# Optimization experiments

Measured on AMD Instinct MI355X. Metric: run time of the kernel, lower is better.

Reference implementation:

```python
import jax, jax.numpy as jnp
import numpy as np

B = 2048
DIMS = [300, 74, 35]
R = 3
ENC = 150
HID = 32
CAT = ENC * R  # 450


def setup_inputs() -> dict:
    key = jax.random.key(0)
    ks = jax.random.split(key, 32)
    d = {}
    for i, dim in enumerate(DIMS):
        d[f"x{i}"] = jax.random.normal(ks[i], (B, 1, dim), dtype=jnp.float32)
    s = 0.05
    for i, dim in enumerate(DIMS):
        d[f"encW{i}"] = jax.random.normal(ks[3 + 2 * i], (ENC, dim), dtype=jnp.float32) * s
        d[f"encb{i}"] = jax.random.normal(ks[4 + 2 * i], (ENC,), dtype=jnp.float32) * s
    d["affw"] = jax.random.normal(ks[10], (R,), dtype=jnp.float32) * s      # Linear(1,1) weight per branch
    d["Ww"] = jax.random.normal(ks[11], (R, HID, 1), dtype=jnp.float32) * s  # Linear(1,32)
    d["Wc"] = jax.random.normal(ks[12], (R, HID, CAT), dtype=jnp.float32) * s  # Linear(450,32)
    d["Wh"] = jax.random.normal(ks[13], (R, 1, HID), dtype=jnp.float32) * s   # Linear(32,1)
    d["clsW1"] = jax.random.normal(ks[14], (128, CAT), dtype=jnp.float32) * s
    d["clsb1"] = jax.random.normal(ks[15], (128,), dtype=jnp.float32) * s
    d["clsW2"] = jax.random.normal(ks[16], (7, 128), dtype=jnp.float32) * s
    d["clsb2"] = jax.random.normal(ks[17], (7,), dtype=jnp.float32) * s
    return d


def reference(x0, x1, x2, encW0, encb0, encW1, encb1, encW2, encb2,
              affw, Ww, Wc, Wh, clsW1, clsb1, clsW2, clsb2):
    xs = [x0, x1, x2]
    encW = [encW0, encW1, encW2]
    encb = [encb0, encb1, encb2]
    # Encode each modality: [B,1,dim_i] -> [B,1,150]
    enc = [jnp.einsum('btd,ed->bte', xs[i], encW[i]) + encb[i] for i in range(R)]
    feat_n = jnp.concatenate(enc, axis=2)            # [B,1,450]
    scale = 1.0 / jnp.sqrt(jnp.float32(feat_n.shape[1]))  # T=1
    att_feats = []
    for i in range(R):
        enc_t = jnp.swapaxes(enc[i], 1, 2)           # [B,150,1]
        t = jnp.swapaxes(feat_n, 1, 2) * affw[i]     # [B,450,1] (Linear(1,1), no bias)
        # outer product attention: [B,150,1] @ [B,1,450] -> [B,150,450]
        att = jnp.tanh(jnp.matmul(enc_t, jnp.swapaxes(t, 1, 2)) * scale)
        a = jnp.einsum('bec,hc->beh', att, Wc[i])    # [B,150,32]
        b = jnp.matmul(enc_t, Ww[i].T)               # [B,150,1]@[1,32] -> [B,150,32]
        H = jax.nn.relu(a + b)
        out_i = jnp.swapaxes(jnp.matmul(H, Wh[i].T), 1, 2) + enc[i]  # [B,1,150]
        att_feats.append(out_i)
    feats = jnp.concatenate(att_feats, axis=2)       # [B,1,450]
    # classifier (dropout is identity in eval mode)
    h = jnp.einsum('btc,kc->btk', feats, clsW1) + clsb1
    return jnp.einsum('btk,ok->bto', h, clsW2) + clsb2
```

## Files before the change

### kernel.cpp

```cpp
#include <hip/hip_runtime.h>
#include <math.h>

#define NJ 5
#define DEG 9
#define X0f 1.25f
#define NB 8
#define NT 768

struct Poly { float c[NJ]; };

#define FMA4(A,S,W) do { (A).x = fmaf((S),(W).x,(A).x); (A).y = fmaf((S),(W).y,(A).y); \
                         (A).z = fmaf((S),(W).z,(A).z); (A).w = fmaf((S),(W).w,(A).w); } while(0)

__global__ __launch_bounds__(256) void k_repack(
    const float* __restrict__ Wc, const float* __restrict__ W1,
    const float* __restrict__ eW0, const float* __restrict__ eW1, const float* __restrict__ eW2,
    float* __restrict__ WcT, float* __restrict__ W1T,
    float* __restrict__ Wt0, float* __restrict__ Wt1, float* __restrict__ Wt2) {
    int tid = blockIdx.x * 256 + threadIdx.x;
    int stride = gridDim.x * 256;
    for (int idx = tid; idx < 3 * 464 * 32; idx += stride) {
        int i = idx / (464 * 32); int rem = idx - i * 464 * 32;
        int m = rem >> 5, h = rem & 31;
        float v = 0.f;
        if (m < 456) {
            int seg = m / 152, e = m - seg * 152;
            if (e < 150) v = Wc[((size_t)i * 32 + h) * 450 + seg * 150 + e];
        }
        WcT[idx] = v;
    }
    for (int idx = tid; idx < 456 * 128; idx += stride) {
        int m = idx >> 7, k = idx & 127;
        int seg = m / 152, e = m - seg * 152;
        W1T[idx] = (e < 150) ? W1[k * 450 + seg * 150 + e] : 0.f;
    }
    for (int idx = tid; idx < 304 * 152; idx += stride) {
        int d = idx / 152, e = idx - d * 152;
        Wt0[idx] = (d < 300 && e < 150) ? eW0[e * 300 + d] : 0.f;
    }
    for (int idx = tid; idx < 76 * 152; idx += stride) {
        int d = idx / 152, e = idx - d * 152;
        Wt1[idx] = (d < 74 && e < 150) ? eW1[e * 74 + d] : 0.f;
    }
    for (int idx = tid; idx < 36 * 152; idx += stride) {
        int d = idx / 152, e = idx - d * 152;
        Wt2[idx] = (d < 35 && e < 150) ? eW2[e * 35 + d] : 0.f;
    }
}

__global__ __launch_bounds__(NT, 1) void k_fused(
    const float* __restrict__ x0, const float* __restrict__ x1, const float* __restrict__ x2,
    const float* __restrict__ eb0, const float* __restrict__ eb1, const float* __restrict__ eb2,
    const float* __restrict__ Wt0, const float* __restrict__ Wt1, const float* __restrict__ Wt2,
    const float* __restrict__ WcT,
    const float* __restrict__ affw, const float* __restrict__ Ww, const float* __restrict__ Wh,
    const float* __restrict__ W1T, const float* __restrict__ cb1,
    const float* __restrict__ cW2, const float* __restrict__ cb2,
    float* __restrict__ out, Poly pc) {
    __shared__ __align__(16) float xs[NB * 428];
    __shared__ __align__(16) float featf[NB * 468];
    __shared__ __align__(16) float fof[NB * 468];
    __shared__ __align__(16) float wWs[96], wHs[96];

    int tid = threadIdx.x;
    int b0 = blockIdx.x * NB;

    if (tid < 96) { wWs[tid] = Ww[tid]; wHs[tid] = Wh[tid]; }
    if (tid >= 96 && tid < 192) {
        int q = tid - 96; int b = q / 12, r = q - b * 12;
        featf[b * 468 + 456 + r] = 0.f;
    }
    if (tid >= 192 && tid < 240) {
        int q = tid - 192; int b = q / 6, r = q - b * 6;
        fof[b * 468 + (r >> 1) * 152 + 150 + (r & 1)] = 0.f;
    }
    for (int idx = tid; idx < NB * 75; idx += NT) {
        int b = idx / 75, q = idx - b * 75;
        ((float4*)(xs + b * 428))[q] = ((const float4*)(x0 + (size_t)(b0 + b) * 300))[q];
    }
    for (int idx = tid; idx < NB * 74; idx += NT) {
        int b = idx / 74, d = idx - b * 74;
        xs[b * 428 + 304 + d] = x1[(size_t)(b0 + b) * 74 + d];
    }
    for (int idx = tid; idx < NB * 35; idx += NT) {
        int b = idx / 35, d = idx - b * 35;
        xs[b * 428 + 380 + d] = x2[(size_t)(b0 + b) * 35 + d];
    }
    __syncthreads();

    {
        int tasks[2]; int nt = 1;
        tasks[0] = tid;
        if (tid >= 624) { tasks[nt++] = 768 + (767 - tid); }
        for (int q = 0; q < nt; ++q) {
            int task = tasks[q];
            int b = task & 7, m4 = task >> 3;
            int seg = (m4 >= 76) ? 2 : (m4 >= 38) ? 1 : 0;
            int e4 = m4 - seg * 38;
            const float* eb = seg == 0 ? eb0 : seg == 1 ? eb1 : eb2;
            const float4* Wt4 = (const float4*)(seg == 0 ? Wt0 : seg == 1 ? Wt1 : Wt2) + e4;
            const float* xb = xs + b * 428 + (seg == 0 ? 0 : seg == 1 ? 304 : 380);
            int DP4 = seg == 0 ? 76 : seg == 1 ? 19 : 9;
            const float4* xr = (const float4*)xb;
            int e = e4 * 4;
            float4 acc;
            acc.x = (e     < 150) ? eb[e]     : 0.f;
            acc.y = (e + 1 < 150) ? eb[e + 1] : 0.f;
            acc.z = (e + 2 < 150) ? eb[e + 2] : 0.f;
            acc.w = (e + 3 < 150) ? eb[e + 3] : 0.f;
            for (int d4 = 0; d4 < DP4; ++d4) {
                float4 x4 = xr[d4];
                float4 w0 = Wt4[(d4 * 4 + 0) * 38];
                float4 w1 = Wt4[(d4 * 4 + 1) * 38];
                float4 w2 = Wt4[(d4 * 4 + 2) * 38];
                float4 w3 = Wt4[(d4 * 4 + 3) * 38];
                FMA4(acc, x4.x, w0);
                FMA4(acc, x4.y, w1);
                FMA4(acc, x4.z, w2);
                FMA4(acc, x4.w, w3);
            }
            ((float4*)(featf + b * 468))[m4] = acc;
        }
    }
    __syncthreads();

    {
        int w = tid >> 6;
        int i = w >> 2, wp = w & 3;
        int lane = tid & 63;
        int hq = lane & 7, slice = (lane >> 3) & 3, bh = lane >> 5;
        int b = wp * 2 + bh;
        float aff = affw[i];
        const float4* Wb4 = (const float4*)WcT + (size_t)i * 3712 + hq;
        const float4* frow = (const float4*)(featf + b * 468);

        float4 acc[NJ];
        #pragma unroll
        for (int J = 0; J < NJ; ++J) acc[J] = make_float4(0.f, 0.f, 0.f, 0.f);
        float mx = 0.f;

        int m4lo = slice * 29;
        #pragma unroll 2
        for (int m4 = m4lo; m4 < m4lo + 29; ++m4) {
            float4 f4 = frow[m4];
            const float4* wp4 = Wb4 + m4 * 32;
            float4 w0 = wp4[0];
            float4 w1 = wp4[8];
            float4 w2 = wp4[16];
            float4 w3 = wp4[24];
            mx = fmaxf(mx, fmaxf(fmaxf(fabsf(f4.x), fabsf(f4.y)), fmaxf(fabsf(f4.z), fabsf(f4.w))));
            float g0 = aff * f4.x, g1 = aff * f4.y, g2 = aff * f4.z, g3 = aff * f4.w;
            float q0 = g0 * g0, q1 = g1 * g1, q2 = g2 * g2, q3 = g3 * g3;
            float p0 = g0, p1 = g1, p2 = g2, p3 = g3;
            FMA4(acc[0], p0, w0); FMA4(acc[0], p1, w1); FMA4(acc[0], p2, w2); FMA4(acc[0], p3, w3);
            #pragma unroll
            for (int J = 1; J < NJ; ++J) {
                p0 *= q0; p1 *= q1; p2 *= q2; p3 *= q3;
                FMA4(acc[J], p0, w0); FMA4(acc[J], p1, w1); FMA4(acc[J], p2, w2); FMA4(acc[J], p3, w3);
            }
        }
        #pragma unroll
        for (int J = 0; J < NJ; ++J) {
            float cJ = pc.c[J];
            float vx = acc[J].x; vx += __shfl_xor(vx, 8); vx += __shfl_xor(vx, 16);
            float vy = acc[J].y; vy += __shfl_xor(vy, 8); vy += __shfl_xor(vy, 16);
            float vz = acc[J].z; vz += __shfl_xor(vz, 8); vz += __shfl_xor(vz, 16);
            float vw = acc[J].w; vw += __shfl_xor(vw, 8); vw += __shfl_xor(vw, 16);
            acc[J].x = vx * cJ; acc[J].y = vy * cJ; acc[J].z = vz * cJ; acc[J].w = vw * cJ;
        }
        mx = fmaxf(mx, __shfl_xor(mx, 1));
        mx = fmaxf(mx, __shfl_xor(mx, 2));
        mx = fmaxf(mx, __shfl_xor(mx, 4));
        mx = fmaxf(mx, __shfl_xor(mx, 8));
        mx = fmaxf(mx, __shfl_xor(mx, 16));
        float gmax = fabsf(aff) * mx;

        float4 wW4 = ((const float4*)wWs)[i * 8 + hq];
        float4 wH4 = ((const float4*)wHs)[i * 8 + hq];
        int e4lo = slice * 10;
        int e4hi = (slice == 3) ? 38 : (e4lo + 10);
        for (int e4 = e4lo; e4 < e4hi; ++e4) {
            float4 s4 = frow[i * 38 + e4];
            float ores[4];
            #pragma unroll
            for (int r = 0; r < 4; ++r) {
                float s = (r == 0) ? s4.x : (r == 1) ? s4.y : (r == 2) ? s4.z : s4.w;
                float4 a4;
                if (fabsf(s) * gmax <= X0f) {
                    float s2 = s * s, p = s;
                    a4.x = acc[0].x * p; a4.y = acc[0].y * p;
                    a4.z = acc[0].z * p; a4.w = acc[0].w * p;
                    #pragma unroll
                    for (int J = 1; J < NJ; ++J) { p *= s2; FMA4(a4, p, acc[J]); }
                } else {
                    a4 = make_float4(0.f, 0.f, 0.f, 0.f);
                    for (int c = 0; c < 456; ++c) {
                        float t = tanhf(s * aff * featf[b * 468 + c]);
                        float4 wv = Wb4[c * 8];
                        FMA4(a4, t, wv);
                    }
                }
                float hx = fmaxf(fmaf(s, wW4.x, a4.x), 0.f);
                float hy = fmaxf(fmaf(s, wW4.y, a4.y), 0.f);
                float hz = fmaxf(fmaf(s, wW4.z, a4.z), 0.f);
                float hw = fmaxf(fmaf(s, wW4.w, a4.w), 0.f);
                float csum = hx * wH4.x + hy * wH4.y + hz * wH4.z + hw * wH4.w;
                csum += __shfl_xor(csum, 1);
                csum += __shfl_xor(csum, 2);
                csum += __shfl_xor(csum, 4);
                ores[r] = csum + s;
            }
            if (hq == 0)
                ((float4*)(fof + b * 468))[i * 38 + e4] = make_float4(ores[0], ores[1], ores[2], ores[3]);
        }
    }
    __syncthreads();

    {
        int cs = tid >> 8;
        int rr = tid & 255;
        int b = rr & 7, k4 = rr >> 3;
        const float4* W14 = (const float4*)W1T + k4;
        const float4* fr = (const float4*)(fof + b * 468);
        float4 a = make_float4(0.f, 0.f, 0.f, 0.f);
        int c4lo = cs * 38;
        for (int c4 = c4lo; c4 < c4lo + 38; ++c4) {
            float4 fv = fr[c4];
            float4 w0 = W14[(c4 * 4 + 0) * 32];
            float4 w1 = W14[(c4 * 4 + 1) * 32];
            float4 w2 = W14[(c4 * 4 + 2) * 32];
            float4 w3 = W14[(c4 * 4 + 3) * 32];
            FMA4(a, fv.x, w0);
            FMA4(a, fv.y, w1);
            FMA4(a, fv.z, w2);
            FMA4(a, fv.w, w3);
        }
        ((float4*)xs)[(cs * 8 + b) * 33 + k4] = a;
    }
    __syncthreads();
    if (tid < 256) {
        int b = tid >> 5, k4 = tid & 31;
        const float4* hp4 = (const float4*)xs;
        float4 v  = hp4[(0 * 8 + b) * 33 + k4];
        float4 v1 = hp4[(1 * 8 + b) * 33 + k4];
        float4 v2 = hp4[(2 * 8 + b) * 33 + k4];
        float4 bias = ((const float4*)cb1)[k4];
        v.x += v1.x + v2.x + bias.x;
        v.y += v1.y + v2.y + bias.y;
        v.z += v1.z + v2.z + bias.z;
        v.w += v1.w + v2.w + bias.w;
        ((float4*)(featf + b * 468))[k4] = v;
    }
    __syncthreads();
    if (tid < NB * 7) {
        int b = tid / 7, o = tid - (tid / 7) * 7;
        const float* hb = featf + b * 468;
        const float* w2 = cW2 + o * 128;
        float acc = cb2[o];
        #pragma unroll 4
        for (int k = 0; k < 128; ++k) acc = fmaf(hb[k], w2[k], acc);
        out[(size_t)(b0 + b) * 7 + o] = acc;
    }
}

static void make_poly(float* cf) {
    const double a = 1.25;
    const int NQ = 128;
    const double PI = 3.14159265358979323846;
    double b[DEG + 1];
    for (int k = 0; k <= DEG; ++k) b[k] = 0.0;
    for (int m = 0; m < NQ; ++m) {
        double th = PI * (m + 0.5) / NQ;
        double f = tanh(a * cos(th));
        for (int k = 1; k <= DEG; k += 2)
            b[k] += (2.0 / NQ) * f * cos(k * th);
    }
    double Tp[DEG + 1], Tc[DEG + 1], Tn[DEG + 1], mono[DEG + 1];
    for (int j = 0; j <= DEG; ++j) { Tp[j] = 0; Tc[j] = 0; mono[j] = 0; }
    Tp[0] = 1.0;
    Tc[1] = 1.0;
    for (int j = 0; j <= DEG; ++j) mono[j] += b[1] * Tc[j];
    for (int k = 2; k <= DEG; ++k) {
        for (int j = 0; j <= DEG; ++j) Tn[j] = -Tp[j];
        for (int j = 1; j <= DEG; ++j) Tn[j] += 2.0 * Tc[j - 1];
        for (int j = 0; j <= DEG; ++j) { Tp[j] = Tc[j]; Tc[j] = Tn[j]; }
        if (k & 1) for (int j = 0; j <= DEG; ++j) mono[j] += b[k] * Tc[j];
    }
    for (int J = 0; J < NJ; ++J) {
        int j = 2 * J + 1;
        cf[J] = (float)(mono[j] / pow(a, (double)j));
    }
}

extern "C" void kernel_launch(void* const* d_in, const int* in_sizes, int n_in,
                              void* d_out, int out_size, void* d_ws, size_t ws_size,
                              hipStream_t stream) {
    (void)in_sizes; (void)n_in; (void)out_size; (void)ws_size;
    const float* x0    = (const float*)d_in[0];
    const float* x1    = (const float*)d_in[1];
    const float* x2    = (const float*)d_in[2];
    const float* eW0   = (const float*)d_in[3];
    const float* eb0   = (const float*)d_in[4];
    const float* eW1   = (const float*)d_in[5];
    const float* eb1   = (const float*)d_in[6];
    const float* eW2   = (const float*)d_in[7];
    const float* eb2   = (const float*)d_in[8];
    const float* affw  = (const float*)d_in[9];
    const float* Ww    = (const float*)d_in[10];
    const float* Wc    = (const float*)d_in[11];
    const float* Wh    = (const float*)d_in[12];
    const float* cW1   = (const float*)d_in[13];
    const float* cb1   = (const float*)d_in[14];
    const float* cW2   = (const float*)d_in[15];
    const float* cb2   = (const float*)d_in[16];

    float* ws    = (float*)d_ws;
    float* wsWcT = ws;
    float* wsW1T = ws + 44544;
    float* wsWt0 = ws + 102912;
    float* wsWt1 = ws + 149120;
    float* wsWt2 = ws + 160672;

    Poly pc;
    make_poly(pc.c);

    k_repack<<<dim3(96), dim3(256), 0, stream>>>(Wc, cW1, eW0, eW1, eW2,
                                                 wsWcT, wsW1T, wsWt0, wsWt1, wsWt2);
    k_fused<<<dim3(256), dim3(NT), 0, stream>>>(x0, x1, x2, eb0, eb1, eb2,
                                                wsWt0, wsWt1, wsWt2, wsWcT,
                                                affw, Ww, Wh, wsW1T, cb1, cW2, cb2,
                                                (float*)d_out, pc);
}
```

Baseline: 67.29 us.

## Share Wc loads across two batch rows and shrink tanh polynomial degree

Each lane in the moment-accumulation loop now processes two batch rows at once, so every loaded Wc weight float4 serves both rows. The feature range is split eight ways instead of four, and an extra shuffle stage reduces across the wider split. The tanh Chebyshev polynomial degree drops from 9 to 7 and the accuracy threshold from 1.25 to 1.1, cutting the accumulator count. The trade-off is more inputs falling back to the exact tanh loop, more register pressure, and some loss of accuracy.

```diff
diff --git a/kernel.cpp b/kernel.cpp
--- a/kernel.cpp
+++ b/kernel.cpp
@@ -1,9 +1,9 @@
 #include <hip/hip_runtime.h>
 #include <math.h>
 
-#define NJ 5
-#define DEG 9
-#define X0f 1.25f
+#define NJ 4
+#define DEG 7
+#define X0f 1.1f
 #define NB 8
 #define NT 768
 
@@ -128,57 +128,93 @@
         int w = tid >> 6;
         int i = w >> 2, wp = w & 3;
         int lane = tid & 63;
-        int hq = lane & 7, slice = (lane >> 3) & 3, bh = lane >> 5;
-        int b = wp * 2 + bh;
+        int hq = lane & 7, slice = lane >> 3;
+        int slice2 = (lane >> 3) & 3, bh = lane >> 5;
         float aff = affw[i];
         const float4* Wb4 = (const float4*)WcT + (size_t)i * 3712 + hq;
-        const float4* frow = (const float4*)(featf + b * 468);
-
-        float4 acc[NJ];
+        int bA = wp * 2, bB = bA + 1;
+        const float4* frowA = (const float4*)(featf + bA * 468);
+        const float4* frowB = (const float4*)(featf + bB * 468);
+
+        float4 accA[NJ], accB[NJ];
         #pragma unroll
-        for (int J = 0; J < NJ; ++J) acc[J] = make_float4(0.f, 0.f, 0.f, 0.f);
-        float mx = 0.f;
-
-        int m4lo = slice * 29;
-        #pragma unroll 2
-        for (int m4 = m4lo; m4 < m4lo + 29; ++m4) {
-            float4 f4 = frow[m4];
+        for (int J = 0; J < NJ; ++J) {
+            accA[J] = make_float4(0.f, 0.f, 0.f, 0.f);
+            accB[J] = make_float4(0.f, 0.f, 0.f, 0.f);
+        }
+        float mxA = 0.f, mxB = 0.f;
+
+        int m4lo = (slice < 4) ? slice * 15 : 60 + (slice - 4) * 14;
+        int m4n  = (slice < 4) ? 15 : 14;
+        #pragma unroll 3
+        for (int k = 0; k < m4n; ++k) {
+            int m4 = m4lo + k;
+            float4 fA = frowA[m4];
+            float4 fB = frowB[m4];
             const float4* wp4 = Wb4 + m4 * 32;
             float4 w0 = wp4[0];
             float4 w1 = wp4[8];
             float4 w2 = wp4[16];
             float4 w3 = wp4[24];
-            mx = fmaxf(mx, fmaxf(fmaxf(fabsf(f4.x), fabsf(f4.y)), fmaxf(fabsf(f4.z), fabsf(f4.w))));
-            float g0 = aff * f4.x, g1 = aff * f4.y, g2 = aff * f4.z, g3 = aff * f4.w;
-            float q0 = g0 * g0, q1 = g1 * g1, q2 = g2 * g2, q3 = g3 * g3;
-            float p0 = g0, p1 = g1, p2 = g2, p3 = g3;
-            FMA4(acc[0], p0, w0); FMA4(acc[0], p1, w1); FMA4(acc[0], p2, w2); FMA4(acc[0], p3, w3);
-            #pragma unroll
-            for (int J = 1; J < NJ; ++J) {
-                p0 *= q0; p1 *= q1; p2 *= q2; p3 *= q3;
-                FMA4(acc[J], p0, w0); FMA4(acc[J], p1, w1); FMA4(acc[J], p2, w2); FMA4(acc[J], p3, w3);
+            mxA = fmaxf(mxA, fmaxf(fmaxf(fabsf(fA.x), fabsf(fA.y)), fmaxf(fabsf(fA.z), fabsf(fA.w))));
+            mxB = fmaxf(mxB, fmaxf(fmaxf(fabsf(fB.x), fabsf(fB.y)), fmaxf(fabsf(fB.z), fabsf(fB.w))));
+            {
+                float g0 = aff * fA.x, g1 = aff * fA.y, g2 = aff * fA.z, g3 = aff * fA.w;
+                float q0 = g0 * g0, q1 = g1 * g1, q2 = g2 * g2, q3 = g3 * g3;
+                float p0 = g0, p1 = g1, p2 = g2, p3 = g3;
+                FMA4(accA[0], p0, w0); FMA4(accA[0], p1, w1); FMA4(accA[0], p2, w2); FMA4(accA[0], p3, w3);
+                #pragma unroll
+                for (int J = 1; J < NJ; ++J) {
+                    p0 *= q0; p1 *= q1; p2 *= q2; p3 *= q3;
+                    FMA4(accA[J], p0, w0); FMA4(accA[J], p1, w1); FMA4(accA[J], p2, w2); FMA4(accA[J], p3, w3);
+                }
+            }
+            {
+                float g0 = aff * fB.x, g1 = aff * fB.y, g2 = aff * fB.z, g3 = aff * fB.w;
+                float q0 = g0 * g0, q1 = g1 * g1, q2 = g2 * g2, q3 = g3 * g3;
+                float p0 = g0, p1 = g1, p2 = g2, p3 = g3;
+                FMA4(accB[0], p0, w0); FMA4(accB[0], p1, w1); FMA4(accB[0], p2, w2); FMA4(accB[0], p3, w3);
+                #pragma unroll
+                for (int J = 1; J < NJ; ++J) {
+                    p0 *= q0; p1 *= q1; p2 *= q2; p3 *= q3;
+                    FMA4(accB[J], p0, w0); FMA4(accB[J], p1, w1); FMA4(accB[J], p2, w2); FMA4(accB[J], p3, w3);
+                }
             }
         }
         #pragma unroll
         for (int J = 0; J < NJ; ++J) {
             float cJ = pc.c[J];
-            float vx = acc[J].x; vx += __shfl_xor(vx, 8); vx += __shfl_xor(vx, 16);
-            float vy = acc[J].y; vy += __shfl_xor(vy, 8); vy += __shfl_xor(vy, 16);
-            float vz = acc[J].z; vz += __shfl_xor(vz, 8); vz += __shfl_xor(vz, 16);
-            float vw = acc[J].w; vw += __shfl_xor(vw, 8); vw += __shfl_xor(vw, 16);
-            acc[J].x = vx * cJ; acc[J].y = vy * cJ; acc[J].z = vz * cJ; acc[J].w = vw * cJ;
-        }
-        mx = fmaxf(mx, __shfl_xor(mx, 1));
-        mx = fmaxf(mx, __shfl_xor(mx, 2));
-        mx = fmaxf(mx, __shfl_xor(mx, 4));
-        mx = fmaxf(mx, __shfl_xor(mx, 8));
-        mx = fmaxf(mx, __shfl_xor(mx, 16));
-        float gmax = fabsf(aff) * mx;
+            float vx, vy, vz, vw;
+            vx = accA[J].x; vx += __shfl_xor(vx, 8); vx += __shfl_xor(vx, 16); vx += __shfl_xor(vx, 32);
+            vy = accA[J].y; vy += __shfl_xor(vy, 8); vy += __shfl_xor(vy, 16); vy += __shfl_xor(vy, 32);
+            vz = accA[J].z; vz += __shfl_xor(vz, 8); vz += __shfl_xor(vz, 16); vz += __shfl_xor(vz, 32);
+            vw = accA[J].w; vw += __shfl_xor(vw, 8); vw += __shfl_xor(vw, 16); vw += __shfl_xor(vw, 32);
+            accA[J].x = vx * cJ; accA[J].y = vy * cJ; accA[J].z = vz * cJ; accA[J].w = vw * cJ;
+            vx = accB[J].x; vx += __shfl_xor(vx, 8); vx += __shfl_xor(vx, 16); vx += __shfl_xor(vx, 32);
+            vy = accB[J].y; vy += __shfl_xor(vy, 8); vy += __shfl_xor(vy, 16); vy += __shfl_xor(vy, 32);
+            vz = accB[J].z; vz += __shfl_xor(vz, 8); vz += __shfl_xor(vz, 16); vz += __shfl_xor(vz, 32);
+            vw = accB[J].w; vw += __shfl_xor(vw, 8); vw += __shfl_xor(vw, 16); vw += __shfl_xor(vw, 32);
+            accB[J].x = vx * cJ; accB[J].y = vy * cJ; accB[J].z = vz * cJ; accB[J].w = vw * cJ;
+        }
+        mxA = fmaxf(mxA, __shfl_xor(mxA, 8));
+        mxA = fmaxf(mxA, __shfl_xor(mxA, 16));
+        mxA = fmaxf(mxA, __shfl_xor(mxA, 32));
+        mxB = fmaxf(mxB, __shfl_xor(mxB, 8));
+        mxB = fmaxf(mxB, __shfl_xor(mxB, 16));
+        mxB = fmaxf(mxB, __shfl_xor(mxB, 32));
+
+        float4 Ms[NJ];
+        #pragma unroll
+        for (int J = 0; J < NJ; ++J) Ms[J] = bh ? accB[J] : accA[J];
+        float gmax = fabsf(aff) * (bh ? mxB : mxA);
+        int b = bA + bh;
+        const float* fb = featf + b * 468;
+        const float4* frow = bh ? frowB : frowA;
 
         float4 wW4 = ((const float4*)wWs)[i * 8 + hq];
         float4 wH4 = ((const float4*)wHs)[i * 8 + hq];
-        int e4lo = slice * 10;
-        int e4hi = (slice == 3) ? 38 : (e4lo + 10);
+        int e4lo = slice2 * 10;
+        int e4hi = (slice2 == 3) ? 38 : (e4lo + 10);
         for (int e4 = e4lo; e4 < e4hi; ++e4) {
             float4 s4 = frow[i * 38 + e4];
             float ores[4];
@@ -188,14 +224,14 @@
                 float4 a4;
                 if (fabsf(s) * gmax <= X0f) {
                     float s2 = s * s, p = s;
-                    a4.x = acc[0].x * p; a4.y = acc[0].y * p;
-                    a4.z = acc[0].z * p; a4.w = acc[0].w * p;
+                    a4.x = Ms[0].x * p; a4.y = Ms[0].y * p;
+                    a4.z = Ms[0].z * p; a4.w = Ms[0].w * p;
                     #pragma unroll
-                    for (int J = 1; J < NJ; ++J) { p *= s2; FMA4(a4, p, acc[J]); }
+                    for (int J = 1; J < NJ; ++J) { p *= s2; FMA4(a4, p, Ms[J]); }
                 } else {
                     a4 = make_float4(0.f, 0.f, 0.f, 0.f);
                     for (int c = 0; c < 456; ++c) {
-                        float t = tanhf(s * aff * featf[b * 468 + c]);
+                        float t = tanhf(s * aff * fb[c]);
                         float4 wv = Wb4[c * 8];
                         FMA4(a4, t, wv);
                     }
@@ -264,7 +300,7 @@
 }
 
 static void make_poly(float* cf) {
-    const double a = 1.25;
+    const double a = 1.1;
     const int NQ = 128;
     const double PI = 3.14159265358979323846;
     double b[DEG + 1];
```

After: 67.33 us. About the same (+0.1%).
